# Performance work log

Hardware: AMD Instinct MI355X
Metric: run time of the kernel (lower is better)

The kernel has to match this reference:

```python
import jax, jax.numpy as jnp
import numpy as np

NEG_SLOPE = 0.2
DROP_RATE = 0.1


def _spmm(rows, cols, vals, x):
    # sparse [N,N] @ dense [N,D] via gather + segment-sum
    n = x.shape[0]
    return jax.ops.segment_sum(vals[:, None] * x[cols], rows, num_segments=n)


def _dropout(x, key, rate=DROP_RATE):
    keep = 1.0 - rate
    mask = jax.random.bernoulli(key, keep, x.shape)
    return jnp.where(mask, x / keep, 0.0).astype(x.dtype)


def _leaky(x):
    return jnp.where(x >= 0, x, NEG_SLOPE * x)


def setup_inputs() -> dict:
    key = jax.random.key(0)
    N, HID, IEMB, NNZ = 100000, 256, 128, 3200000
    ks = jax.random.split(key, 8)
    x_idx = jnp.arange(N, dtype=jnp.int32)
    embed_weight = jax.random.normal(ks[0], (N, HID), jnp.float32) * 0.02
    G_rows = jax.random.randint(ks[1], (NNZ,), 0, N, jnp.int32)
    G_cols = jax.random.randint(ks[2], (NNZ,), 0, N, jnp.int32)
    G_vals = jax.random.uniform(ks[3], (NNZ,), jnp.float32) / 32.0
    W1 = jax.random.normal(ks[4], (HID, HID), jnp.float32) * (1.0 / np.sqrt(HID))
    b1 = jnp.zeros((HID,), jnp.float32)
    W2 = jax.random.normal(ks[5], (HID, HID), jnp.float32) * (1.0 / np.sqrt(HID))
    b2 = jnp.zeros((HID,), jnp.float32)
    W3 = jax.random.normal(ks[6], (IEMB, HID), jnp.float32) * (1.0 / np.sqrt(HID))
    b3 = jnp.zeros((IEMB,), jnp.float32)
    return {"x_idx": x_idx, "embed_weight": embed_weight,
            "G_rows": G_rows, "G_cols": G_cols, "G_vals": G_vals,
            "W1": W1, "b1": b1, "W2": W2, "b2": b2, "W3": W3, "b3": b3}


def reference(x_idx, embed_weight, G_rows, G_cols, G_vals, W1, b1, W2, b2, W3, b3):
    dk = jax.random.split(jax.random.key(42), 3)
    x = embed_weight[x_idx]                                   # [N, HID]
    m1 = _dropout(_spmm(G_rows, G_cols, G_vals, x) + x, dk[0])
    x1 = _leaky(m1 @ W1.T + b1)
    m2 = _dropout(_spmm(G_rows, G_cols, G_vals, x1) + x1, dk[1])
    x2 = _leaky(m2 @ W2.T + b2)
    m3 = _dropout(_spmm(G_rows, G_cols, G_vals, x2) + x2, dk[2])
    x3 = _leaky(m3 @ W3.T + b3)
    return jnp.concatenate((x, x1, x2, x3), axis=1)          # [N, 3*HID+IEMB]
```

## Files before the change

kernel.cpp:

```cpp
#include <hip/hip_runtime.h>
#include <stdint.h>
#include <stddef.h>

static constexpr int N    = 100000;
static constexpr int HID  = 256;
static constexpr int IEMB = 128;
static constexpr int NNZ  = 3200000;
static constexpr int OUTW = 3 * HID + IEMB;
static constexpr float NEG_SLOPE = 0.2f;

#define THREEFRY_PARTITIONABLE 1

typedef __attribute__((ext_vector_type(8))) short bf16x8;
typedef __attribute__((ext_vector_type(4))) float f32x4;
typedef __attribute__((ext_vector_type(4))) unsigned short us4;

__host__ __device__ inline uint32_t rotl32(uint32_t v, int r) {
  return (v << r) | (v >> (32 - r));
}

__host__ __device__ inline void threefry2x32(uint32_t k0, uint32_t k1,
                                             uint32_t x0, uint32_t x1,
                                             uint32_t& o0, uint32_t& o1) {
  const uint32_t k2 = k0 ^ k1 ^ 0x1BD11BDAu;
  x0 += k0; x1 += k1;
  x0 += x1; x1 = rotl32(x1, 13); x1 ^= x0;
  x0 += x1; x1 = rotl32(x1, 15); x1 ^= x0;
  x0 += x1; x1 = rotl32(x1, 26); x1 ^= x0;
  x0 += x1; x1 = rotl32(x1,  6); x1 ^= x0;
  x0 += k1; x1 += k2 + 1u;
  x0 += x1; x1 = rotl32(x1, 17); x1 ^= x0;
  x0 += x1; x1 = rotl32(x1, 29); x1 ^= x0;
  x0 += x1; x1 = rotl32(x1, 16); x1 ^= x0;
  x0 += x1; x1 = rotl32(x1, 24); x1 ^= x0;
  x0 += k2; x1 += k0 + 2u;
  x0 += x1; x1 = rotl32(x1, 13); x1 ^= x0;
  x0 += x1; x1 = rotl32(x1, 15); x1 ^= x0;
  x0 += x1; x1 = rotl32(x1, 26); x1 ^= x0;
  x0 += x1; x1 = rotl32(x1,  6); x1 ^= x0;
  x0 += k0; x1 += k1 + 3u;
  x0 += x1; x1 = rotl32(x1, 17); x1 ^= x0;
  x0 += x1; x1 = rotl32(x1, 29); x1 ^= x0;
  x0 += x1; x1 = rotl32(x1, 16); x1 ^= x0;
  x0 += x1; x1 = rotl32(x1, 24); x1 ^= x0;
  x0 += k1; x1 += k2 + 4u;
  x0 += x1; x1 = rotl32(x1, 13); x1 ^= x0;
  x0 += x1; x1 = rotl32(x1, 15); x1 ^= x0;
  x0 += x1; x1 = rotl32(x1, 26); x1 ^= x0;
  x0 += x1; x1 = rotl32(x1,  6); x1 ^= x0;
  x0 += k2; x1 += k0 + 5u;
  o0 = x0; o1 = x1;
}

__device__ inline bool keep_elem(uint32_t k0, uint32_t k1, uint32_t e) {
  uint32_t o0, o1, bits;
#if THREEFRY_PARTITIONABLE
  threefry2x32(k0, k1, 0u, e, o0, o1);
  bits = o0 ^ o1;
#else
  const uint32_t H = (uint32_t)(N) * (uint32_t)(HID) / 2u;
  if (e < H) { threefry2x32(k0, k1, e, e + H, o0, o1); bits = o0; }
  else       { threefry2x32(k0, k1, e - H, e, o0, o1); bits = o1; }
#endif
  float u = __uint_as_float((bits >> 9) | 0x3f800000u) - 1.0f;
  return u < 0.9f;
}

__device__ inline unsigned short f2bf_rne(float x) {
  uint32_t u = __float_as_uint(x);
  uint32_t r = (u + 0x7FFFu + ((u >> 16) & 1u)) >> 16;
  return (unsigned short)r;
}
__device__ inline float bf2f(unsigned short h) {
  return __uint_as_float(((uint32_t)h) << 16);
}


__global__ __launch_bounds__(256) void k_gather(const int* __restrict__ xidx,
                                                const float* __restrict__ emb,
                                                float* __restrict__ A,
                                                unsigned short* __restrict__ Abf,
                                                float* __restrict__ out) {
  int t = blockIdx.x * 256 + threadIdx.x;
  int n = t >> 6;
  int c4 = (t & 63) * 4;
  if (n >= N) return;
  int src = xidx[n];
  float4 v = *(const float4*)(emb + (size_t)src * HID + c4);
  *(float4*)(out + (size_t)n * OUTW + c4) = v;
  *(float4*)(A + (size_t)n * HID + c4) = v;
  if (Abf) {
    us4 q;
    q[0] = f2bf_rne(v.x); q[1] = f2bf_rne(v.y);
    q[2] = f2bf_rne(v.z); q[3] = f2bf_rne(v.w);
    *(us4*)(Abf + (size_t)n * HID + c4) = q;
  }
}

__global__ __launch_bounds__(256) void k_zero(float4* __restrict__ p, int n4) {
  int i = blockIdx.x * 256 + threadIdx.x;
  if (i < n4) p[i] = make_float4(0.f, 0.f, 0.f, 0.f);
}

__global__ __launch_bounds__(256) void k_zero_i(int* __restrict__ p, int n) {
  int i = blockIdx.x * 256 + threadIdx.x;
  if (i < n) p[i] = 0;
}

__global__ __launch_bounds__(256) void k_wsplit(const float* __restrict__ W,
                                                unsigned short* __restrict__ whi,
                                                unsigned short* __restrict__ wlo,
                                                int n) {
  int i = blockIdx.x * 256 + threadIdx.x;
  if (i >= n) return;
  float w = W[i];
  unsigned short h = f2bf_rne(w);
  unsigned short l = f2bf_rne(w - bf2f(h));
  whi[i] = h; wlo[i] = l;
}


__global__ __launch_bounds__(256) void k_hist(const int* __restrict__ rows,
                                              int* __restrict__ RO) {
  int e = blockIdx.x * 256 + threadIdx.x;
  if (e < NNZ) atomicAdd(&RO[rows[e]], 1);
}

__global__ __launch_bounds__(256) void k_scan(int* __restrict__ RO, int* __restrict__ C) {
  __shared__ int part[256];
  const int T = 256;
  const int K = (N + T - 1) / T;
  int t = threadIdx.x;
  int lo = t * K;
  int hi = lo + K; if (hi > N) hi = N;
  int s = 0;
  for (int i = lo; i < hi; ++i) s += RO[i];
  part[t] = s;
  __syncthreads();
  if (t == 0) {
    int run = 0;
    for (int i = 0; i < T; ++i) { int v = part[i]; part[i] = run; run += v; }
  }
  __syncthreads();
  int run = part[t];
  for (int i = lo; i < hi; ++i) {
    int v = RO[i];
    RO[i] = run;
    C[i]  = run;
    run += v;
  }
  if (t == T - 1) RO[N] = run;
}

__global__ __launch_bounds__(256) void k_scatter(const int* __restrict__ rows,
                                                 const int* __restrict__ cols,
                                                 const float* __restrict__ vals,
                                                 int* __restrict__ C,
                                                 int2* __restrict__ CV) {
  int e = blockIdx.x * 256 + threadIdx.x;
  if (e >= NNZ) return;
  int r = rows[e];
  int pos = atomicAdd(&C[r], 1);
  CV[pos] = make_int2(cols[e], __float_as_int(vals[e]));
}

template <bool BF>
__global__ __launch_bounds__(256) void k_spmm_csr(const int* __restrict__ RO,
                                                  const int2* __restrict__ CV,
                                                  const float* __restrict__ A,
                                                  const unsigned short* __restrict__ Abf,
                                                  float* __restrict__ B,
                                                  uint32_t k0, uint32_t k1) {
  int r = blockIdx.x * 4 + (threadIdx.x >> 6);
  if (r >= N) return;
  int c4 = (threadIdx.x & 63) * 4;
  int beg = RO[r], end = RO[r + 1];

  float4 res = *(const float4*)(A + (size_t)r * HID + c4);
  uint32_t e0 = (uint32_t)r * (uint32_t)HID + (uint32_t)c4;
  bool kp0 = keep_elem(k0, k1, e0 + 0u);
  bool kp1 = keep_elem(k0, k1, e0 + 1u);
  bool kp2 = keep_elem(k0, k1, e0 + 2u);
  bool kp3 = keep_elem(k0, k1, e0 + 3u);

  float ax = 0.f, ay = 0.f, az = 0.f, aw = 0.f;
  int i = beg;

  if (BF) {
#pragma unroll 1
    for (; i + 7 < end; i += 8) {
      int2 cv[8];
#pragma unroll
      for (int u = 0; u < 8; ++u) cv[u] = CV[i + u];
      us4 q[8];
#pragma unroll
      for (int u = 0; u < 8; ++u)
        q[u] = *(const us4*)(Abf + (size_t)cv[u].x * HID + c4);
#pragma unroll
      for (int u = 0; u < 8; ++u) {
        float v = __int_as_float(cv[u].y);
        ax = fmaf(v, bf2f(q[u][0]), ax);
        ay = fmaf(v, bf2f(q[u][1]), ay);
        az = fmaf(v, bf2f(q[u][2]), az);
        aw = fmaf(v, bf2f(q[u][3]), aw);
      }
    }
    for (; i < end; ++i) {
      int2 cv = CV[i];
      float v = __int_as_float(cv.y);
      us4 q = *(const us4*)(Abf + (size_t)cv.x * HID + c4);
      ax = fmaf(v, bf2f(q[0]), ax);
      ay = fmaf(v, bf2f(q[1]), ay);
      az = fmaf(v, bf2f(q[2]), az);
      aw = fmaf(v, bf2f(q[3]), aw);
    }
  } else {
#pragma unroll 1
    for (; i + 3 < end; i += 4) {
      int2 cv0 = CV[i + 0], cv1 = CV[i + 1], cv2 = CV[i + 2], cv3 = CV[i + 3];
      float4 x0 = *(const float4*)(A + (size_t)cv0.x * HID + c4);
      float4 x1 = *(const float4*)(A + (size_t)cv1.x * HID + c4);
      float4 x2 = *(const float4*)(A + (size_t)cv2.x * HID + c4);
      float4 x3 = *(const float4*)(A + (size_t)cv3.x * HID + c4);
      float v0 = __int_as_float(cv0.y), v1 = __int_as_float(cv1.y);
      float v2 = __int_as_float(cv2.y), v3 = __int_as_float(cv3.y);
      ax = fmaf(v0, x0.x, ax); ay = fmaf(v0, x0.y, ay);
      az = fmaf(v0, x0.z, az); aw = fmaf(v0, x0.w, aw);
      ax = fmaf(v1, x1.x, ax); ay = fmaf(v1, x1.y, ay);
      az = fmaf(v1, x1.z, az); aw = fmaf(v1, x1.w, aw);
      ax = fmaf(v2, x2.x, ax); ay = fmaf(v2, x2.y, ay);
      az = fmaf(v2, x2.z, az); aw = fmaf(v2, x2.w, aw);
      ax = fmaf(v3, x3.x, ax); ay = fmaf(v3, x3.y, ay);
      az = fmaf(v3, x3.z, az); aw = fmaf(v3, x3.w, aw);
    }
    for (; i < end; ++i) {
      int2 cv = CV[i];
      float v = __int_as_float(cv.y);
      float4 x = *(const float4*)(A + (size_t)cv.x * HID + c4);
      ax = fmaf(v, x.x, ax); ay = fmaf(v, x.y, ay);
      az = fmaf(v, x.z, az); aw = fmaf(v, x.w, aw);
    }
  }

  float4 o;
  o.x = kp0 ? (ax + res.x) / 0.9f : 0.0f;
  o.y = kp1 ? (ay + res.y) / 0.9f : 0.0f;
  o.z = kp2 ? (az + res.z) / 0.9f : 0.0f;
  o.w = kp3 ? (aw + res.w) / 0.9f : 0.0f;
  *(float4*)(B + (size_t)r * HID + c4) = o;
}

template <int NC, bool WRITE_F32>
__global__ __launch_bounds__(256) void k_gemm_mfma(const float* __restrict__ M,
                                                   const unsigned short* __restrict__ Whi,
                                                   const unsigned short* __restrict__ Wlo,
                                                   const float* __restrict__ bias,
                                                   float* __restrict__ Aout,
                                                   unsigned short* __restrict__ Abf,
                                                   float* __restrict__ out,
                                                   int colbase) {
  constexpr int WC = NC / 4;
  constexpr int CT = WC / 16;
  __shared__ __align__(16) unsigned short mhi[64 * 128];
  __shared__ __align__(16) unsigned short mlo[64 * 128];

  const int tid  = threadIdx.x;
  const int wave = tid >> 6;
  const int lane = tid & 63;
  const int l15  = lane & 15;
  const int lhi  = lane >> 4;
  const int row0 = blockIdx.x * 64;
  const int wc0  = wave * WC;

  const f32x4 fzero = {0.f, 0.f, 0.f, 0.f};
  f32x4 acc[4][CT];
#pragma unroll
  for (int rt = 0; rt < 4; ++rt)
#pragma unroll
    for (int ct = 0; ct < CT; ++ct) acc[rt][ct] = fzero;

  const int tk = (tid & 31) * 4;
  const int tr = tid >> 5;

#pragma unroll 1
  for (int kc = 0; kc < HID; kc += 128) {
    __syncthreads();
#pragma unroll
    for (int p = 0; p < 8; ++p) {
      int r = p * 8 + tr;
      int grow = row0 + r;
      float4 v = make_float4(0.f, 0.f, 0.f, 0.f);
      if (grow < N) v = *(const float4*)(M + (size_t)grow * HID + kc + tk);
      float vv[4] = {v.x, v.y, v.z, v.w};
      us4 h, l;
#pragma unroll
      for (int c = 0; c < 4; ++c) {
        unsigned short hh = f2bf_rne(vv[c]);
        h[c] = hh;
        l[c] = f2bf_rne(vv[c] - bf2f(hh));
      }
      int sidx = r * 128 + (tk ^ ((r & 7) << 3));
      *(us4*)(&mhi[sidx]) = h;
      *(us4*)(&mlo[sidx]) = l;
    }
    __syncthreads();

#pragma unroll
    for (int ks = 0; ks < 128; ks += 32) {
      const int kf = ks + lhi * 8;
      bf16x8 ah[4], al[4];
#pragma unroll
      for (int rt = 0; rt < 4; ++rt) {
        int r = rt * 16 + l15;
        int idx = r * 128 + (kf ^ ((r & 7) << 3));
        ah[rt] = *(const bf16x8*)(&mhi[idx]);
        al[rt] = *(const bf16x8*)(&mlo[idx]);
      }
#pragma unroll
      for (int ct = 0; ct < CT; ++ct) {
        int col = wc0 + ct * 16 + l15;
        const unsigned short* wph = Whi + (size_t)col * HID + kc + kf;
        const unsigned short* wpl = Wlo + (size_t)col * HID + kc + kf;
        bf16x8 bh = *(const bf16x8*)wph;
        bf16x8 bl = *(const bf16x8*)wpl;
#pragma unroll
        for (int rt = 0; rt < 4; ++rt) {
          acc[rt][ct] = __builtin_amdgcn_mfma_f32_16x16x32_bf16(ah[rt], bh, acc[rt][ct], 0, 0, 0);
          acc[rt][ct] = __builtin_amdgcn_mfma_f32_16x16x32_bf16(ah[rt], bl, acc[rt][ct], 0, 0, 0);
          acc[rt][ct] = __builtin_amdgcn_mfma_f32_16x16x32_bf16(al[rt], bh, acc[rt][ct], 0, 0, 0);
        }
      }
    }
  }

#pragma unroll
  for (int ct = 0; ct < CT; ++ct) {
    int col = wc0 + ct * 16 + l15;
    float bv = bias[col];
#pragma unroll
    for (int rt = 0; rt < 4; ++rt) {
#pragma unroll
      for (int rg = 0; rg < 4; ++rg) {
        int grow = row0 + rt * 16 + lhi * 4 + rg;
        if (grow < N) {
          float v = acc[rt][ct][rg] + bv;
          v = (v >= 0.f) ? v : NEG_SLOPE * v;
          out[(size_t)grow * OUTW + colbase + col] = v;
          if (WRITE_F32) {
            Aout[(size_t)grow * HID + col] = v;
            if (Abf) Abf[(size_t)grow * HID + col] = f2bf_rne(v);
          }
        }
      }
    }
  }
}

__global__ __launch_bounds__(256) void k_spmm(const int* __restrict__ rows,
                                              const int* __restrict__ cols,
                                              const float* __restrict__ vals,
                                              const float* __restrict__ A,
                                              float* __restrict__ B) {
  int e = blockIdx.x * 4 + (threadIdx.x >> 6);
  int lane = threadIdx.x & 63;
  if (e >= NNZ) return;
  int r = rows[e];
  int c = cols[e];
  float v = vals[e];
  float4 x = *(const float4*)(A + (size_t)c * HID + lane * 4);
  float* bp = B + (size_t)r * HID + lane * 4;
  unsafeAtomicAdd(bp + 0, v * x.x);
  unsafeAtomicAdd(bp + 1, v * x.y);
  unsafeAtomicAdd(bp + 2, v * x.z);
  unsafeAtomicAdd(bp + 3, v * x.w);
}

__global__ __launch_bounds__(256) void k_dropres(const float* __restrict__ A,
                                                 float* __restrict__ B,
                                                 uint32_t k0, uint32_t k1) {
  uint32_t e = blockIdx.x * 256 + threadIdx.x;
  if (e >= (uint32_t)N * HID) return;
  float m = B[e] + A[e];
  B[e] = keep_elem(k0, k1, e) ? (m / 0.9f) : 0.0f;
}

template <int NC, bool WRITE_F32>
__global__ __launch_bounds__(256) void k_gemm(const float* __restrict__ M,
                                              const float* __restrict__ W,
                                              const float* __restrict__ bias,
                                              float* __restrict__ Aout,
                                              float* __restrict__ out,
                                              int colbase) {
  constexpr int CG = NC / 4;
  constexpr int RG = 256 / CG;
  constexpr int RPT = 64 / RG;
  __shared__ float m_s[64][68];

  const int tid = threadIdx.x;
  const int j = tid % CG;
  const int rg = tid / CG;
  const int row0 = blockIdx.x * 64;
  const int r0 = rg * RPT;

  float acc[RPT][4];
#pragma unroll
  for (int i = 0; i < RPT; ++i)
#pragma unroll
    for (int c = 0; c < 4; ++c) acc[i][c] = 0.f;

  const int rr = tid >> 4;
  const int kk = (tid & 15) * 4;

#pragma unroll 1
  for (int kc = 0; kc < HID; kc += 64) {
    __syncthreads();
#pragma unroll
    for (int p = 0; p < 4; ++p) {
      int r = p * 16 + rr;
      int grow = row0 + r;
      float4 v = make_float4(0.f, 0.f, 0.f, 0.f);
      if (grow < N) v = *(const float4*)(M + (size_t)grow * HID + kc + kk);
      m_s[kk + 0][r] = v.x;
      m_s[kk + 1][r] = v.y;
      m_s[kk + 2][r] = v.z;
      m_s[kk + 3][r] = v.w;
    }
    __syncthreads();

#pragma unroll 1
    for (int ks = 0; ks < 64; ks += 8) {
      float4 wa[4], wb[4];
#pragma unroll
      for (int c = 0; c < 4; ++c) {
        const float* wp = W + (size_t)(4 * j + c) * HID + kc + ks;
        wa[c] = *(const float4*)(wp);
        wb[c] = *(const float4*)(wp + 4);
      }
#pragma unroll
      for (int q = 0; q < 8; ++q) {
        float wf[4];
#pragma unroll
        for (int c = 0; c < 4; ++c) {
          const float* wv = (q < 4) ? (const float*)&wa[c] : (const float*)&wb[c];
          wf[c] = wv[q & 3];
        }
        const float* ms = &m_s[ks + q][r0];
#pragma unroll
        for (int ii = 0; ii < RPT / 4; ++ii) {
          float4 mv = *(const float4*)(ms + ii * 4);
          const float mr[4] = {mv.x, mv.y, mv.z, mv.w};
#pragma unroll
          for (int t = 0; t < 4; ++t)
#pragma unroll
            for (int c = 0; c < 4; ++c)
              acc[ii * 4 + t][c] = fmaf(mr[t], wf[c], acc[ii * 4 + t][c]);
        }
      }
    }
  }

  float bv[4];
#pragma unroll
  for (int c = 0; c < 4; ++c) bv[c] = bias[4 * j + c];

#pragma unroll
  for (int i = 0; i < RPT; ++i) {
    int grow = row0 + r0 + i;
    if (grow < N) {
      float4 ov;
      float* ovp = (float*)&ov;
#pragma unroll
      for (int c = 0; c < 4; ++c) {
        float v = acc[i][c] + bv[c];
        ovp[c] = (v >= 0.f) ? v : NEG_SLOPE * v;
      }
      if (WRITE_F32)
        *(float4*)(Aout + (size_t)grow * HID + 4 * j) = ov;
      *(float4*)(out + (size_t)grow * OUTW + colbase + 4 * j) = ov;
    }
  }
}

extern "C" void kernel_launch(void* const* d_in, const int* in_sizes, int n_in,
                              void* d_out, int out_size, void* d_ws, size_t ws_size,
                              hipStream_t stream) {
  (void)in_sizes; (void)n_in; (void)out_size;

  const int*   x_idx  = (const int*)d_in[0];
  const float* emb    = (const float*)d_in[1];
  const int*   g_rows = (const int*)d_in[2];
  const int*   g_cols = (const int*)d_in[3];
  const float* g_vals = (const float*)d_in[4];
  const float* W1 = (const float*)d_in[5];
  const float* b1 = (const float*)d_in[6];
  const float* W2 = (const float*)d_in[7];
  const float* b2 = (const float*)d_in[8];
  const float* W3 = (const float*)d_in[9];
  const float* b3 = (const float*)d_in[10];
  float* out = (float*)d_out;

  float* A = (float*)d_ws;
  float* B = A + (size_t)N * HID;
  int*   RO = (int*)(B + (size_t)N * HID);
  int*   C  = RO + (N + 2);
  int2*  CV = (int2*)(C + N);
  uintptr_t wsp = ((uintptr_t)(CV + NNZ) + 63) & ~(uintptr_t)63;
  unsigned short* Wh0 = (unsigned short*)wsp;
  unsigned short* Wl0 = Wh0 + 65536;
  unsigned short* Wh1 = Wl0 + 65536;
  unsigned short* Wl1 = Wh1 + 65536;
  unsigned short* Wh2 = Wl1 + 65536;
  unsigned short* Wl2 = Wh2 + 32768;
  unsigned short* Abf = Wl2 + 32768;
  const size_t NEED_CSR = (size_t)N * HID * 2 * sizeof(float)
                        + (size_t)(N + 2 + N) * sizeof(int)
                        + (size_t)NNZ * sizeof(int2)
                        + 64
                        + (size_t)(4 * 65536 + 2 * 32768) * sizeof(unsigned short);
  const size_t NEED_BF = NEED_CSR + (size_t)N * HID * sizeof(unsigned short);
  const bool use_csr = (ws_size >= NEED_CSR);
  const bool use_bf  = (ws_size >= NEED_BF);
  unsigned short* AbfArg = use_bf ? Abf : nullptr;

  uint32_t dk[3][2];
#if THREEFRY_PARTITIONABLE
  for (uint32_t i = 0; i < 3; ++i)
    threefry2x32(0u, 42u, 0u, i, dk[i][0], dk[i][1]);
#else
  {
    uint32_t a0, c0, a1, c1, a2, c2;
    threefry2x32(0u, 42u, 0u, 3u, a0, c0);
    threefry2x32(0u, 42u, 1u, 4u, a1, c1);
    threefry2x32(0u, 42u, 2u, 5u, a2, c2);
    dk[0][0] = a0; dk[0][1] = a1;
    dk[1][0] = a2; dk[1][1] = c0;
    dk[2][0] = c1; dk[2][1] = c2;
  }
#endif

  const int gemm_blocks = (N + 63) / 64;

  k_gather<<<(N * 64) / 256, 256, 0, stream>>>(x_idx, emb, A, AbfArg, out);

  const float* Ws[3] = {W1, W2, W3};
  const float* bs[3] = {b1, b2, b3};
  unsigned short* Whs[3] = {Wh0, Wh1, Wh2};
  unsigned short* Wls[3] = {Wl0, Wl1, Wl2};

  if (use_csr) {
    k_zero_i<<<(N + 2 + 255) / 256, 256, 0, stream>>>(RO, N + 2);
    k_hist<<<(NNZ + 255) / 256, 256, 0, stream>>>(g_rows, RO);
    k_scan<<<1, 256, 0, stream>>>(RO, C);
    k_scatter<<<(NNZ + 255) / 256, 256, 0, stream>>>(g_rows, g_cols, g_vals, C, CV);
    k_wsplit<<<(65536 + 255) / 256, 256, 0, stream>>>(W1, Wh0, Wl0, 65536);
    k_wsplit<<<(65536 + 255) / 256, 256, 0, stream>>>(W2, Wh1, Wl1, 65536);
    k_wsplit<<<(32768 + 255) / 256, 256, 0, stream>>>(W3, Wh2, Wl2, 32768);
  }

  for (int l = 0; l < 3; ++l) {
    if (use_csr) {
      if (use_bf)
        k_spmm_csr<true><<<(N + 3) / 4, 256, 0, stream>>>(RO, CV, A, Abf, B, dk[l][0], dk[l][1]);
      else
        k_spmm_csr<false><<<(N + 3) / 4, 256, 0, stream>>>(RO, CV, A, nullptr, B, dk[l][0], dk[l][1]);
      if (l < 2)
        k_gemm_mfma<HID, true><<<gemm_blocks, 256, 0, stream>>>(B, Whs[l], Wls[l], bs[l], A, AbfArg, out, HID * (l + 1));
      else
        k_gemm_mfma<IEMB, false><<<gemm_blocks, 256, 0, stream>>>(B, Whs[2], Wls[2], bs[2], nullptr, nullptr, out, 3 * HID);
    } else {
      k_zero<<<(N * HID / 4 + 255) / 256, 256, 0, stream>>>((float4*)B, N * HID / 4);
      k_spmm<<<NNZ / 4, 256, 0, stream>>>(g_rows, g_cols, g_vals, A, B);
      k_dropres<<<(N * HID) / 256, 256, 0, stream>>>(A, B, dk[l][0], dk[l][1]);
      if (l < 2)
        k_gemm<HID, true><<<gemm_blocks, 256, 0, stream>>>(B, Ws[l], bs[l], A, out, HID * (l + 1));
      else
        k_gemm<IEMB, false><<<gemm_blocks, 256, 0, stream>>>(B, Ws[2], bs[2], nullptr, out, 3 * HID);
    }
  }
}
```

Measured before the change: 2.277 ms.

## Prepack weights into MFMA fragment order and vectorize GEMM epilogue stores

Weight split kernel now writes hi/lo bf16 weights pre-arranged in per-lane MFMA fragment order, so each wave loads contiguous 16-byte fragments instead of strided rows. The MFMA operands are swapped (weights as A, activations as B), which transposes the accumulator layout so each lane holds four consecutive columns. The epilogue then issues float4 and us4 stores with a float4 bias load. This targets uncoalesced weight loads and scalar strided output writes in the GEMM, at the cost of a more complex index mapping.

```diff
diff --git a/kernel.cpp b/kernel.cpp
--- a/kernel.cpp
+++ b/kernel.cpp
@@ -107,16 +107,37 @@
   if (i < n) p[i] = 0;
 }
 
-__global__ __launch_bounds__(256) void k_wsplit(const float* __restrict__ W,
-                                                unsigned short* __restrict__ whi,
-                                                unsigned short* __restrict__ wlo,
-                                                int n) {
-  int i = blockIdx.x * 256 + threadIdx.x;
-  if (i >= n) return;
-  float w = W[i];
-  unsigned short h = f2bf_rne(w);
-  unsigned short l = f2bf_rne(w - bf2f(h));
-  whi[i] = h; wlo[i] = l;
+__global__ __launch_bounds__(256) void k_wsplit_frag(const float* __restrict__ W,
+                                                     unsigned short* __restrict__ whi,
+                                                     unsigned short* __restrict__ wlo,
+                                                     int nct) {
+  int t = blockIdx.x * 256 + threadIdx.x;
+  int total = 8 * nct * 64;
+  if (t >= total) return;
+  int kb   = t / (nct * 64);
+  int rem  = t - kb * nct * 64;
+  int c16  = rem >> 6;
+  int lane = rem & 63;
+  int col  = c16 * 16 + (lane & 15);
+  int kbase = kb * 32 + ((lane >> 4) << 3);
+  const float* wp = W + (size_t)col * HID + kbase;
+  us4 h0, h1, l0, l1;
+#pragma unroll
+  for (int j = 0; j < 4; ++j) {
+    float w = wp[j];
+    unsigned short hh = f2bf_rne(w);
+    h0[j] = hh; l0[j] = f2bf_rne(w - bf2f(hh));
+  }
+#pragma unroll
+  for (int j = 0; j < 4; ++j) {
+    float w = wp[4 + j];
+    unsigned short hh = f2bf_rne(w);
+    h1[j] = hh; l1[j] = f2bf_rne(w - bf2f(hh));
+  }
+  *(us4*)(whi + (size_t)t * 8)     = h0;
+  *(us4*)(whi + (size_t)t * 8 + 4) = h1;
+  *(us4*)(wlo + (size_t)t * 8)     = l0;
+  *(us4*)(wlo + (size_t)t * 8 + 4) = l1;
 }
 
 
@@ -252,15 +273,16 @@
 
 template <int NC, bool WRITE_F32>
 __global__ __launch_bounds__(256) void k_gemm_mfma(const float* __restrict__ M,
-                                                   const unsigned short* __restrict__ Whi,
-                                                   const unsigned short* __restrict__ Wlo,
+                                                   const unsigned short* __restrict__ Whf,
+                                                   const unsigned short* __restrict__ Wlf,
                                                    const float* __restrict__ bias,
                                                    float* __restrict__ Aout,
                                                    unsigned short* __restrict__ Abf,
                                                    float* __restrict__ out,
                                                    int colbase) {
-  constexpr int WC = NC / 4;
-  constexpr int CT = WC / 16;
+  constexpr int WC  = NC / 4;
+  constexpr int CT  = WC / 16;
+  constexpr int NCT = NC / 16;
   __shared__ __align__(16) unsigned short mhi[64 * 128];
   __shared__ __align__(16) unsigned short mlo[64 * 128];
 
@@ -308,26 +330,29 @@
 #pragma unroll
     for (int ks = 0; ks < 128; ks += 32) {
       const int kf = ks + lhi * 8;
-      bf16x8 ah[4], al[4];
+      bf16x8 mh[4], ml[4];
 #pragma unroll
       for (int rt = 0; rt < 4; ++rt) {
         int r = rt * 16 + l15;
         int idx = r * 128 + (kf ^ ((r & 7) << 3));
-        ah[rt] = *(const bf16x8*)(&mhi[idx]);
-        al[rt] = *(const bf16x8*)(&mlo[idx]);
-      }
+        mh[rt] = *(const bf16x8*)(&mhi[idx]);
+        ml[rt] = *(const bf16x8*)(&mlo[idx]);
+      }
+      const int kbg = (kc + ks) >> 5;
+      bf16x8 wh[CT], wl[CT];
 #pragma unroll
       for (int ct = 0; ct < CT; ++ct) {
-        int col = wc0 + ct * 16 + l15;
-        const unsigned short* wph = Whi + (size_t)col * HID + kc + kf;
-        const unsigned short* wpl = Wlo + (size_t)col * HID + kc + kf;
-        bf16x8 bh = *(const bf16x8*)wph;
-        bf16x8 bl = *(const bf16x8*)wpl;
+        size_t wfo = ((size_t)(kbg * NCT + wave * CT + ct) * 64 + lane) * 8;
+        wh[ct] = *(const bf16x8*)(Whf + wfo);
+        wl[ct] = *(const bf16x8*)(Wlf + wfo);
+      }
+#pragma unroll
+      for (int ct = 0; ct < CT; ++ct) {
 #pragma unroll
         for (int rt = 0; rt < 4; ++rt) {
-          acc[rt][ct] = __builtin_amdgcn_mfma_f32_16x16x32_bf16(ah[rt], bh, acc[rt][ct], 0, 0, 0);
-          acc[rt][ct] = __builtin_amdgcn_mfma_f32_16x16x32_bf16(ah[rt], bl, acc[rt][ct], 0, 0, 0);
-          acc[rt][ct] = __builtin_amdgcn_mfma_f32_16x16x32_bf16(al[rt], bh, acc[rt][ct], 0, 0, 0);
+          acc[rt][ct] = __builtin_amdgcn_mfma_f32_16x16x32_bf16(wh[ct], mh[rt], acc[rt][ct], 0, 0, 0);
+          acc[rt][ct] = __builtin_amdgcn_mfma_f32_16x16x32_bf16(wh[ct], ml[rt], acc[rt][ct], 0, 0, 0);
+          acc[rt][ct] = __builtin_amdgcn_mfma_f32_16x16x32_bf16(wl[ct], mh[rt], acc[rt][ct], 0, 0, 0);
         }
       }
     }
@@ -335,20 +360,28 @@
 
 #pragma unroll
   for (int ct = 0; ct < CT; ++ct) {
-    int col = wc0 + ct * 16 + l15;
-    float bv = bias[col];
+    int colq = wc0 + ct * 16 + lhi * 4;
+    float4 bv = *(const float4*)(bias + colq);
+    const float* bvp = (const float*)&bv;
 #pragma unroll
     for (int rt = 0; rt < 4; ++rt) {
-#pragma unroll
-      for (int rg = 0; rg < 4; ++rg) {
-        int grow = row0 + rt * 16 + lhi * 4 + rg;
-        if (grow < N) {
-          float v = acc[rt][ct][rg] + bv;
-          v = (v >= 0.f) ? v : NEG_SLOPE * v;
-          out[(size_t)grow * OUTW + colbase + col] = v;
-          if (WRITE_F32) {
-            Aout[(size_t)grow * HID + col] = v;
-            if (Abf) Abf[(size_t)grow * HID + col] = f2bf_rne(v);
+      int grow = row0 + rt * 16 + l15;
+      if (grow < N) {
+        float4 ov;
+        float* ovp = (float*)&ov;
+#pragma unroll
+        for (int c = 0; c < 4; ++c) {
+          float v = acc[rt][ct][c] + bvp[c];
+          ovp[c] = (v >= 0.f) ? v : NEG_SLOPE * v;
+        }
+        *(float4*)(out + (size_t)grow * OUTW + colbase + colq) = ov;
+        if (WRITE_F32) {
+          *(float4*)(Aout + (size_t)grow * HID + colq) = ov;
+          if (Abf) {
+            us4 q;
+            q[0] = f2bf_rne(ov.x); q[1] = f2bf_rne(ov.y);
+            q[2] = f2bf_rne(ov.z); q[3] = f2bf_rne(ov.w);
+            *(us4*)(Abf + (size_t)grow * HID + colq) = q;
           }
         }
       }
@@ -552,9 +585,9 @@
     k_hist<<<(NNZ + 255) / 256, 256, 0, stream>>>(g_rows, RO);
     k_scan<<<1, 256, 0, stream>>>(RO, C);
     k_scatter<<<(NNZ + 255) / 256, 256, 0, stream>>>(g_rows, g_cols, g_vals, C, CV);
-    k_wsplit<<<(65536 + 255) / 256, 256, 0, stream>>>(W1, Wh0, Wl0, 65536);
-    k_wsplit<<<(65536 + 255) / 256, 256, 0, stream>>>(W2, Wh1, Wl1, 65536);
-    k_wsplit<<<(32768 + 255) / 256, 256, 0, stream>>>(W3, Wh2, Wl2, 32768);
+    k_wsplit_frag<<<(8 * 16 * 64 + 255) / 256, 256, 0, stream>>>(W1, Wh0, Wl0, 16);
+    k_wsplit_frag<<<(8 * 16 * 64 + 255) / 256, 256, 0, stream>>>(W2, Wh1, Wl1, 16);
+    k_wsplit_frag<<<(8 * 8 * 64 + 255) / 256, 256, 0, stream>>>(W3, Wh2, Wl2, 8);
   }
 
   for (int l = 0; l < 3; ++l) {
```

Result: no change. 2.241 ms (-1.6%).
